# Optimization experiments

Hardware: AMD Instinct MI355X
Metric: run time of the kernel (lower is better)

## Reference

```python
import jax, jax.numpy as jnp
import numpy as np

D = 512      # emb_size
H = 8        # attention heads
E = 8        # num experts
HID = 512    # expert MLP hidden (assumed StandardExpert = 2-layer MLP)
NTOK = 8192  # 8*1024 tokens
W_IMP = 0.01


def setup_inputs() -> dict:
    key = jax.random.key(0)
    ks = jax.random.split(key, 16)
    f = lambda i, shape, s=0.02: (jax.random.normal(ks[i], shape, jnp.float32) * s)
    return {
        "x": jax.random.normal(ks[0], (8, 1024, D), jnp.float32),
        "q": jax.random.normal(ks[1], (NTOK, D), jnp.float32),
        "Wq": f(2, (D, D)), "bq": jnp.zeros((D,), jnp.float32),
        "Wk": f(3, (D, D)), "bk": jnp.zeros((D,), jnp.float32),
        "Wv": f(4, (D, D)), "bv": jnp.zeros((D,), jnp.float32),
        "Wo": f(5, (D, D)), "bo": jnp.zeros((D,), jnp.float32),
        "gate_W": f(6, (D, E)), "gate_b": jnp.zeros((E,), jnp.float32),
        "W1": f(7, (E, D, HID)), "b1": jnp.zeros((E, HID), jnp.float32),
        "W2": f(8, (E, HID, D)), "b2": jnp.zeros((E, D), jnp.float32),
        "top": 2,
    }


def _cross_att(xf, q, Wq, bq, Wk, bk, Wv, bv, Wo, bo):
    # seq_len == 1 on both sides after unsqueeze(1) in the torch code
    N, d = xf.shape
    dh = d // H
    Q = (xf @ Wq + bq).reshape(N, H, dh)
    K = (q @ Wk + bk).reshape(N, H, dh)
    V = (q @ Wv + bv).reshape(N, H, dh)
    scores = jnp.sum(Q * K, axis=-1, keepdims=True) / jnp.sqrt(jnp.float32(dh))  # [N,H,1]
    w = jax.nn.softmax(scores, axis=-1)  # trivially ones (single key), kept for fidelity
    att = (w * V).reshape(N, d)
    return att @ Wo + bo


def reference(x, q, Wq, bq, Wk, bk, Wv, bv, Wo, bo, gate_W, gate_b, W1, b1, W2, b2, top):
    x_shape = x.shape
    xf = x.reshape(-1, x_shape[-1])  # [N, D]
    att = _cross_att(xf, q, Wq, bq, Wk, bk, Wv, bv, Wo, bo)
    gate_logits = att @ gate_W + gate_b
    gate_prob = jax.nn.softmax(gate_logits, axis=-1)  # [N, E] (eval mode: no noise)
    top_w, top_i = jax.lax.top_k(gate_prob, top)       # [N, top]
    top_w = jax.nn.softmax(top_w, axis=-1)
    # combine weights per expert: comb[n,e] = sum_k top_w[n,k] * [top_i[n,k]==e]
    comb = jnp.sum(top_w[..., None] * jax.nn.one_hot(top_i, E, dtype=xf.dtype), axis=1)  # [N, E]
    y = jnp.zeros_like(xf)
    for e in range(E):  # fixed small expert loop; dense compute + mask-combine
        h = jax.nn.relu(xf @ W1[e] + b1[e])
        ye = h @ W2[e] + b2[e]
        y = y + comb[:, e:e + 1] * ye
    importance = gate_prob.sum(axis=0)  # [E]
    # torch.std uses ddof=1
    importance_loss = W_IMP * (jnp.std(importance, ddof=1) / jnp.mean(importance)) ** 2
    return y.reshape(x_shape), gate_prob, importance_loss
```

## Files before the change

kernel.cpp:

```cpp
#include <hip/hip_runtime.h>
#include <math.h>
#include <stdint.h>

#define NTOK 8192
#define DIM  512
#define NEXP 8
#define HIDN 512
#define BM 128
#define BN 128
#define BK 32
#define MAXRB 72
#define SLOTS (MAXRB*BM)
#define GBLK (NTOK/16)

typedef _Float16 f16;
typedef __attribute__((ext_vector_type(4))) _Float16 f16x4;
typedef __attribute__((ext_vector_type(8))) _Float16 f16x8;
typedef __attribute__((ext_vector_type(4))) float    f32x4;

__device__ __forceinline__ void gl2lds16(const void* g, void* l) {
  __builtin_amdgcn_global_load_lds(
      (const __attribute__((address_space(1))) unsigned int*)(g),
      (__attribute__((address_space(3))) unsigned int*)(l), 16, 0, 0);
}

__global__ __launch_bounds__(256) void k_prep(
    const float* __restrict__ x, f16* __restrict__ xh,
    const float* __restrict__ W1, const float* __restrict__ W2,
    f16* __restrict__ W1t, f16* __restrict__ W2t) {
  const int bx = blockIdx.x, tid = threadIdx.x;
  if (bx < 4096) {
    int i4 = (bx * 256 + tid) * 4;
    float4 v = *(const float4*)(x + i4);
    f16x4 o; o.x = (_Float16)v.x; o.y = (_Float16)v.y; o.z = (_Float16)v.z; o.w = (_Float16)v.w;
    *(f16x4*)(xh + i4) = o;
  } else {
    __shared__ float t[32][33];
    int idx = bx - 4096;
    int z = idx >> 8, rem = idx & 255;
    int k0 = (rem >> 4) * 32, n0 = (rem & 15) * 32;
    const float* src = (z < 8 ? W1 : W2) + (size_t)(z & 7) * DIM * DIM;
    f16* dst = (z < 8 ? W1t : W2t) + (size_t)(z & 7) * DIM * DIM;
    int tx = tid & 31, ty = tid >> 5;
    for (int r = ty; r < 32; r += 8) t[r][tx] = src[(size_t)(k0 + r) * DIM + n0 + tx];
    __syncthreads();
    for (int r = ty; r < 32; r += 8) dst[(size_t)(n0 + r) * DIM + k0 + tx] = (f16)t[tx][r];
  }
}

__global__ void k_foldA(const float* __restrict__ Wo, const float* __restrict__ gW,
                        double* __restrict__ G1) {
  int out = blockIdx.x * 4 + (threadIdx.x >> 6);
  int lane = threadIdx.x & 63;
  int d = out >> 3, e = out & 7;
  double acc = 0.0;
#pragma unroll
  for (int j = 0; j < 8; j++) {
    int k = j * 64 + lane;
    acc += (double)Wo[d * DIM + k] * (double)gW[k * NEXP + e];
  }
#pragma unroll
  for (int off = 32; off; off >>= 1) acc += __shfl_xor(acc, off, 64);
  if (lane == 0) G1[out] = acc;
}

__global__ void k_foldB(const float* __restrict__ Wv, const double* __restrict__ G1,
                        float* __restrict__ Wg, const float* __restrict__ bv,
                        const float* __restrict__ bo, const float* __restrict__ gW,
                        const float* __restrict__ gb, double* __restrict__ bg) {
  int lane = threadIdx.x & 63;
  if (blockIdx.x == 1024) {
    int w = threadIdx.x >> 6;
    for (int e = w; e < NEXP; e += 4) {
      double acc = 0.0;
#pragma unroll
      for (int j = 0; j < 8; j++) {
        int d = j * 64 + lane;
        acc += (double)bv[d] * G1[d * NEXP + e] + (double)bo[d] * (double)gW[d * NEXP + e];
      }
#pragma unroll
      for (int off = 32; off; off >>= 1) acc += __shfl_xor(acc, off, 64);
      if (lane == 0) bg[e] = acc + (double)gb[e];
    }
    return;
  }
  int out = blockIdx.x * 4 + (threadIdx.x >> 6);
  int d = out >> 3, e = out & 7;
  double acc = 0.0;
#pragma unroll
  for (int j = 0; j < 8; j++) {
    int k = j * 64 + lane;
    acc += (double)Wv[d * DIM + k] * G1[k * NEXP + e];
  }
#pragma unroll
  for (int off = 32; off; off >>= 1) acc += __shfl_xor(acc, off, 64);
  if (lane == 0) Wg[out] = (float)acc;
}

__global__ __launch_bounds__(256) void k_gate(
    const float* __restrict__ q, const float* __restrict__ Wg,
    const double* __restrict__ bg, float* __restrict__ gp_out,
    int* __restrict__ e1a, int* __restrict__ e2a,
    float* __restrict__ w1a, float* __restrict__ w2a,
    int* __restrict__ r1a, int* __restrict__ r2a, int* __restrict__ hist,
    float* __restrict__ gpsum) {
  __shared__ float qs[16 * 513];
  __shared__ float ps[16][8];
  __shared__ int cnt[16];
  const int tid = threadIdx.x;
  const int tok0 = blockIdx.x * 16;

  for (int i = tid; i < 16 * 512; i += 256) {
    int r = i >> 9, c = i & 511;
    qs[r * 513 + c] = q[(size_t)(tok0 + r) * DIM + c];
  }
  if (tid < 16) cnt[tid] = 0;
  __syncthreads();

  const int e = tid & 7;
  const int half = (tid >> 3) & 1;
  const int tl = tid >> 4;
  const float* qrow = qs + tl * 513 + half * 256;
  const float* wcol = Wg + half * 256 * NEXP + e;

  double a0 = 0, a1 = 0, a2 = 0, a3 = 0;
#pragma unroll 4
  for (int j = 0; j < 256; j += 4) {
    a0 += (double)qrow[j]     * (double)wcol[(size_t)j * NEXP];
    a1 += (double)qrow[j + 1] * (double)wcol[(size_t)(j + 1) * NEXP];
    a2 += (double)qrow[j + 2] * (double)wcol[(size_t)(j + 2) * NEXP];
    a3 += (double)qrow[j + 3] * (double)wcol[(size_t)(j + 3) * NEXP];
  }
  double acc = (a0 + a1) + (a2 + a3);
  acc += __shfl_xor(acc, 8, 64);

  double l = acc + bg[e];
  double m = l;
#pragma unroll
  for (int off = 1; off < 8; off <<= 1) m = fmax(m, __shfl_xor(m, off, 64));
  float ex = expf((float)(l - m));
  float s = ex;
#pragma unroll
  for (int off = 1; off < 8; off <<= 1) s += __shfl_xor(s, off, 64);
  float pf = ex / s;
  int tok = tok0 + tl;
  if (half == 0) { gp_out[(size_t)tok * NEXP + e] = pf; ps[tl][e] = pf; }

  double v1 = l; int i1 = e;
#pragma unroll
  for (int off = 1; off < 8; off <<= 1) {
    double ov = __shfl_xor(v1, off, 64);
    int oi = __shfl_xor(i1, off, 64);
    if (ov > v1 || (ov == v1 && oi < i1)) { v1 = ov; i1 = oi; }
  }
  double v2 = (e == i1) ? -1e300 : l; int i2 = e;
#pragma unroll
  for (int off = 1; off < 8; off <<= 1) {
    double ov = __shfl_xor(v2, off, 64);
    int oi = __shfl_xor(i2, off, 64);
    if (ov > v2 || (ov == v2 && oi < i2)) { v2 = ov; i2 = oi; }
  }
  float p1 = __shfl(pf, (tl << 4) + i1, 64);
  float p2 = __shfl(pf, (tl << 4) + i2, 64);
  if (e == 0 && half == 0) {
    float ev = expf(p2 - p1);
    float iw = 1.0f / (1.0f + ev);
    e1a[tok] = i1; e2a[tok] = i2;
    w1a[tok] = iw; w2a[tok] = ev * iw;
    r1a[tok] = atomicAdd(&cnt[i1], 1);
    r2a[tok] = atomicAdd(&cnt[8 + i2], 1);
  }
  __syncthreads();
  if (tid < 16) hist[blockIdx.x * 16 + tid] = cnt[tid];
  if (tid < 8) {
    float ssum = 0.f;
#pragma unroll
    for (int r = 0; r < 16; r++) ssum += ps[r][tid];
    gpsum[blockIdx.x * 8 + tid] = ssum;
  }
}

__global__ __launch_bounds__(1024) void k_scan2(const int* __restrict__ hist,
                                                int* __restrict__ blockbase,
                                                int* __restrict__ aoff,
                                                int* __restrict__ counts,
                                                int* __restrict__ toks,
                                                const float* __restrict__ gpsum,
                                                float* __restrict__ loss) {
  __shared__ int tot[16];
  __shared__ int s_ao[16];
  __shared__ double imp[8];
  const int c = threadIdx.x >> 6;
  const int l = threadIdx.x & 63;
  int v[GBLK / 64];
  int s = 0;
#pragma unroll
  for (int j = 0; j < GBLK / 64; j++) {
    v[j] = hist[((l * (GBLK / 64) + j) << 4) + c];
    s += v[j];
  }
  int incl = s;
#pragma unroll
  for (int off = 1; off < 64; off <<= 1) {
    int t = __shfl_up(incl, off, 64);
    if (l >= off) incl += t;
  }
  int run = incl - s;
#pragma unroll
  for (int j = 0; j < GBLK / 64; j++) {
    blockbase[((l * (GBLK / 64) + j) << 4) + c] = run;
    run += v[j];
  }
  if (l == 63) tot[c] = incl;
  __syncthreads();
  if (threadIdx.x == 0) {
    int o0 = 0, o1 = 0;
    for (int e = 0; e < NEXP; e++) {
      counts[e] = tot[e];
      aoff[e] = o0; s_ao[e] = o0; o0 += (tot[e] + BM - 1) / BM * BM;
      counts[8 + e] = tot[8 + e];
      aoff[9 + e] = o1; s_ao[8 + e] = o1; o1 += (tot[8 + e] + BM - 1) / BM * BM;
    }
    aoff[8] = o0; aoff[17] = o1;
  }
  __syncthreads();
  const int cnt_c = tot[c];
  const int padded = (cnt_c + BM - 1) / BM * BM;
  const int base = ((c >> 3) ? SLOTS : 0) + s_ao[c];
  for (int sidx = cnt_c + l; sidx < padded; sidx += 64)
    toks[base + sidx] = 0;
  if (c < 8) {
    double a = 0.0;
#pragma unroll
    for (int j = 0; j < GBLK / 64; j++)
      a += (double)gpsum[(size_t)(l + j * 64) * 8 + c];
#pragma unroll
    for (int off = 32; off; off >>= 1) a += __shfl_xor(a, off, 64);
    if (l == 0) imp[c] = a;
  }
  __syncthreads();
  if (threadIdx.x == 0) {
    double mn = 0.0;
    for (int e = 0; e < 8; e++) mn += imp[e];
    mn *= (1.0 / 8.0);
    double var = 0.0;
    for (int e = 0; e < 8; e++) { double d = imp[e] - mn; var += d * d; }
    var *= (1.0 / 7.0);
    double r = sqrt(var) / mn;
    loss[0] = (float)(0.01 * r * r);
  }
}

__global__ void k_scatter2(const int* __restrict__ e1a, const int* __restrict__ e2a,
                           const float* __restrict__ w1a, const float* __restrict__ w2a,
                           const int* __restrict__ r1a, const int* __restrict__ r2a,
                           const int* __restrict__ blockbase, const int* __restrict__ aoff,
                           int* __restrict__ toks, float* __restrict__ wsl) {
  int n = blockIdx.x * 256 + threadIdx.x;
  int blk = n >> 4;
  int e1 = e1a[n];
  int slot = aoff[e1] + blockbase[(blk << 4) + e1] + r1a[n];
  toks[slot] = n; wsl[slot] = w1a[n];
  int e2 = e2a[n];
  slot = SLOTS + aoff[9 + e2] + blockbase[(blk << 4) + 8 + e2] + r2a[n];
  toks[slot] = n; wsl[slot] = w2a[n];
}

template <int MODE>
__global__ __launch_bounds__(256) void k_expert(
    const f16* __restrict__ Asrc, const f16* __restrict__ Wt,
    const float* __restrict__ bias, const int* __restrict__ toks,
    const float* __restrict__ wsl, const int* __restrict__ aoff,
    const int* __restrict__ counts, f16* __restrict__ Hout,
    float* __restrict__ y) {
  const int klist = (MODE == 0) ? blockIdx.z : (MODE == 2 ? 1 : 0);
  const int* ao = aoff + klist * 9;
  const int slot0 = blockIdx.x * BM;
  if (slot0 >= ao[8]) return;
  int e = 0;
#pragma unroll
  for (int t = 1; t <= 7; t++) if (slot0 >= ao[t]) e = t;

  const int n0 = blockIdx.y * BN;
  const int tid = threadIdx.x, lane = tid & 63, wid = tid >> 6;

  __shared__ __align__(16) f16 As[BM * BK];
  __shared__ __align__(16) f16 Bs[BN * BK];

  const int srow = wid * 16 + (lane >> 2);
  const int scol = (lane & 3) * 8;
  const f16* arow[2];
  const f16* brow[2];
  f16* alds[2];
  f16* blds[2];
#pragma unroll
  for (int rnd = 0; rnd < 2; rnd++) {
    int r = srow + rnd * 64;
    if (MODE == 0) {
      int tk = toks[klist * SLOTS + slot0 + r];
      arow[rnd] = Asrc + (size_t)tk * DIM + scol;
    } else {
      arow[rnd] = Asrc + (size_t)(klist * SLOTS + slot0 + r) * HIDN + scol;
    }
    brow[rnd] = Wt + ((size_t)e * DIM + n0 + r) * DIM + scol;
    alds[rnd] = As + (wid * 16 + rnd * 64) * BK;
    blds[rnd] = Bs + (wid * 16 + rnd * 64) * BK;
  }

  f32x4 acc[4][4] = {};
  const int wr = wid >> 1, wc = wid & 1;
  const int fr = lane & 15, kb = (lane >> 4) * 8;

  for (int ks = 0; ks < DIM; ks += BK) {
    __syncthreads();
#pragma unroll
    for (int rnd = 0; rnd < 2; rnd++) {
      gl2lds16(arow[rnd] + ks, alds[rnd]);
      gl2lds16(brow[rnd] + ks, blds[rnd]);
    }
    __syncthreads();
    f16x8 af[4], bf[4];
#pragma unroll
    for (int m = 0; m < 4; m++)
      af[m] = *(const f16x8*)(As + (wr * 64 + m * 16 + fr) * BK + kb);
#pragma unroll
    for (int n = 0; n < 4; n++)
      bf[n] = *(const f16x8*)(Bs + (wc * 64 + n * 16 + fr) * BK + kb);
#pragma unroll
    for (int m = 0; m < 4; m++)
#pragma unroll
      for (int n = 0; n < 4; n++)
        acc[m][n] = __builtin_amdgcn_mfma_f32_16x16x32_f16(af[m], bf[n], acc[m][n], 0, 0, 0);
  }

  float bcol[4];
#pragma unroll
  for (int n = 0; n < 4; n++)
    bcol[n] = bias[e * ((MODE == 0) ? HIDN : DIM) + n0 + wc * 64 + n * 16 + fr];

  if (MODE == 0) {
#pragma unroll
    for (int m = 0; m < 4; m++)
#pragma unroll
      for (int r4 = 0; r4 < 4; r4++) {
        int slot = slot0 + wr * 64 + m * 16 + (lane >> 4) * 4 + r4;
#pragma unroll
        for (int n = 0; n < 4; n++) {
          int col = n0 + wc * 64 + n * 16 + fr;
          float v = acc[m][n][r4] + bcol[n];
          Hout[(size_t)(klist * SLOTS + slot) * HIDN + col] = (f16)fmaxf(v, 0.f);
        }
      }
  } else {
    const int vend = ao[e] + counts[klist * 8 + e];
#pragma unroll
    for (int m = 0; m < 4; m++)
#pragma unroll
      for (int r4 = 0; r4 < 4; r4++) {
        int slot = slot0 + wr * 64 + m * 16 + (lane >> 4) * 4 + r4;
        if (slot < vend) {
          int tk = toks[klist * SLOTS + slot];
          float w = wsl[klist * SLOTS + slot];
#pragma unroll
          for (int n = 0; n < 4; n++) {
            int col = n0 + wc * 64 + n * 16 + fr;
            float v = (acc[m][n][r4] + bcol[n]) * w;
            size_t oi = (size_t)tk * DIM + col;
            if (MODE == 1) y[oi] = v;
            else y[oi] += v;
          }
        }
      }
  }
}

extern "C" void kernel_launch(void* const* d_in, const int* in_sizes, int n_in,
                              void* d_out, int out_size, void* d_ws, size_t ws_size,
                              hipStream_t stream) {
  const float* x  = (const float*)d_in[0];
  const float* q  = (const float*)d_in[1];
  const float* Wv = (const float*)d_in[6];
  const float* bv = (const float*)d_in[7];
  const float* Wo = (const float*)d_in[8];
  const float* bo = (const float*)d_in[9];
  const float* gW = (const float*)d_in[10];
  const float* gb = (const float*)d_in[11];
  const float* W1 = (const float*)d_in[12];
  const float* b1 = (const float*)d_in[13];
  const float* W2 = (const float*)d_in[14];
  const float* b2 = (const float*)d_in[15];

  float* out = (float*)d_out;
  float* y_out = out;
  float* gp_out = out + (size_t)NTOK * DIM;
  float* loss_out = gp_out + (size_t)NTOK * NEXP;

  uint8_t* w = (uint8_t*)d_ws;
  size_t o = 0;
  auto alloc = [&](size_t bytes) -> void* {
    void* p = w + o;
    o = (o + bytes + 255) & ~(size_t)255;
    return p;
  };
  f16* xh      = (f16*)alloc((size_t)NTOK * DIM * 2);
  f16* W1t     = (f16*)alloc((size_t)NEXP * DIM * HIDN * 2);
  f16* W2t     = (f16*)alloc((size_t)NEXP * DIM * HIDN * 2);
  f16* Hbuf    = (f16*)alloc((size_t)2 * SLOTS * HIDN * 2);
  double* G1   = (double*)alloc((size_t)DIM * NEXP * 8);
  float* Wg    = (float*)alloc((size_t)DIM * NEXP * 4);
  double* bg   = (double*)alloc(NEXP * 8);
  int* e1a     = (int*)alloc(NTOK * 4);
  int* e2a     = (int*)alloc(NTOK * 4);
  float* w1a   = (float*)alloc(NTOK * 4);
  float* w2a   = (float*)alloc(NTOK * 4);
  int* r1a     = (int*)alloc(NTOK * 4);
  int* r2a     = (int*)alloc(NTOK * 4);
  int* hist    = (int*)alloc((size_t)GBLK * 16 * 4);
  int* bbase   = (int*)alloc((size_t)GBLK * 16 * 4);
  float* gpsum = (float*)alloc((size_t)GBLK * 8 * 4);
  int* counts  = (int*)alloc(16 * 4);
  int* aoff    = (int*)alloc(18 * 4);
  int* toks    = (int*)alloc((size_t)2 * SLOTS * 4);
  float* wsl   = (float*)alloc((size_t)2 * SLOTS * 4);
  (void)ws_size; (void)in_sizes; (void)n_in; (void)out_size;

  k_prep<<<8192, 256, 0, stream>>>(x, xh, W1, W2, W1t, W2t);
  k_foldA<<<1024, 256, 0, stream>>>(Wo, gW, G1);
  k_foldB<<<1025, 256, 0, stream>>>(Wv, G1, Wg, bv, bo, gW, gb, bg);
  k_gate<<<GBLK, 256, 0, stream>>>(q, Wg, bg, gp_out, e1a, e2a, w1a, w2a, r1a, r2a, hist, gpsum);
  k_scan2<<<1, 1024, 0, stream>>>(hist, bbase, aoff, counts, toks, gpsum, loss_out);
  k_scatter2<<<NTOK / 256, 256, 0, stream>>>(e1a, e2a, w1a, w2a, r1a, r2a, bbase, aoff, toks, wsl);
  k_expert<0><<<dim3(MAXRB, 4, 2), 256, 0, stream>>>(xh, W1t, b1, toks, wsl, aoff, counts,
                                                     Hbuf, nullptr);
  k_expert<1><<<dim3(MAXRB, 4, 1), 256, 0, stream>>>(Hbuf, W2t, b2, toks, wsl, aoff, counts,
                                                     nullptr, y_out);
  k_expert<2><<<dim3(MAXRB, 4, 1), 256, 0, stream>>>(Hbuf, W2t, b2, toks, wsl, aoff, counts,
                                                     nullptr, y_out);
}
```

Before: 116.7 us.

## Use k-chunked LDS layout with BK=64, transposed MFMA, vectorized epilogue, fuse foldA

```diff
diff --git a/kernel.cpp b/kernel.cpp
--- a/kernel.cpp
+++ b/kernel.cpp
@@ -8,7 +8,7 @@
 #define HIDN 512
 #define BM 128
 #define BN 128
-#define BK 32
+#define BK 64
 #define MAXRB 72
 #define SLOTS (MAXRB*BM)
 #define GBLK (NTOK/16)
@@ -27,14 +27,16 @@
 __global__ __launch_bounds__(256) void k_prep(
     const float* __restrict__ x, f16* __restrict__ xh,
     const float* __restrict__ W1, const float* __restrict__ W2,
-    f16* __restrict__ W1t, f16* __restrict__ W2t) {
+    f16* __restrict__ W1t, f16* __restrict__ W2t,
+    const float* __restrict__ Wo, const float* __restrict__ gW,
+    double* __restrict__ G1) {
   const int bx = blockIdx.x, tid = threadIdx.x;
   if (bx < 4096) {
     int i4 = (bx * 256 + tid) * 4;
     float4 v = *(const float4*)(x + i4);
     f16x4 o; o.x = (_Float16)v.x; o.y = (_Float16)v.y; o.z = (_Float16)v.z; o.w = (_Float16)v.w;
     *(f16x4*)(xh + i4) = o;
-  } else {
+  } else if (bx < 8192) {
     __shared__ float t[32][33];
     int idx = bx - 4096;
     int z = idx >> 8, rem = idx & 255;
@@ -45,23 +47,20 @@
     for (int r = ty; r < 32; r += 8) t[r][tx] = src[(size_t)(k0 + r) * DIM + n0 + tx];
     __syncthreads();
     for (int r = ty; r < 32; r += 8) dst[(size_t)(n0 + r) * DIM + k0 + tx] = (f16)t[tx][r];
-  }
-}
-
-__global__ void k_foldA(const float* __restrict__ Wo, const float* __restrict__ gW,
-                        double* __restrict__ G1) {
-  int out = blockIdx.x * 4 + (threadIdx.x >> 6);
-  int lane = threadIdx.x & 63;
-  int d = out >> 3, e = out & 7;
-  double acc = 0.0;
-#pragma unroll
-  for (int j = 0; j < 8; j++) {
-    int k = j * 64 + lane;
-    acc += (double)Wo[d * DIM + k] * (double)gW[k * NEXP + e];
-  }
-#pragma unroll
-  for (int off = 32; off; off >>= 1) acc += __shfl_xor(acc, off, 64);
-  if (lane == 0) G1[out] = acc;
+  } else {
+    int out = (bx - 8192) * 4 + (tid >> 6);
+    int lane = tid & 63;
+    int d = out >> 3, e = out & 7;
+    double acc = 0.0;
+#pragma unroll
+    for (int j = 0; j < 8; j++) {
+      int k = j * 64 + lane;
+      acc += (double)Wo[d * DIM + k] * (double)gW[k * NEXP + e];
+    }
+#pragma unroll
+    for (int off = 32; off; off >>= 1) acc += __shfl_xor(acc, off, 64);
+    if (lane == 0) G1[out] = acc;
+  }
 }
 
 __global__ void k_foldB(const float* __restrict__ Wv, const double* __restrict__ G1,
@@ -284,93 +283,104 @@
   const int n0 = blockIdx.y * BN;
   const int tid = threadIdx.x, lane = tid & 63, wid = tid >> 6;
 
-  __shared__ __align__(16) f16 As[BM * BK];
-  __shared__ __align__(16) f16 Bs[BN * BK];
-
-  const int srow = wid * 16 + (lane >> 2);
-  const int scol = (lane & 3) * 8;
-  const f16* arow[2];
-  const f16* brow[2];
-  f16* alds[2];
-  f16* blds[2];
-#pragma unroll
-  for (int rnd = 0; rnd < 2; rnd++) {
-    int r = srow + rnd * 64;
+  __shared__ __align__(16) f16 As[8 * 128 * 8];
+  __shared__ __align__(16) f16 Bs[8 * 128 * 8];
+
+  const f16* abase[2];
+  const f16* bbase[2];
+#pragma unroll
+  for (int half = 0; half < 2; half++) {
+    int row = half * 64 + lane;
     if (MODE == 0) {
-      int tk = toks[klist * SLOTS + slot0 + r];
-      arow[rnd] = Asrc + (size_t)tk * DIM + scol;
+      int tk = toks[klist * SLOTS + slot0 + row];
+      abase[half] = Asrc + (size_t)tk * DIM;
     } else {
-      arow[rnd] = Asrc + (size_t)(klist * SLOTS + slot0 + r) * HIDN + scol;
-    }
-    brow[rnd] = Wt + ((size_t)e * DIM + n0 + r) * DIM + scol;
-    alds[rnd] = As + (wid * 16 + rnd * 64) * BK;
-    blds[rnd] = Bs + (wid * 16 + rnd * 64) * BK;
+      abase[half] = Asrc + (size_t)(klist * SLOTS + slot0 + row) * HIDN;
+    }
+    bbase[half] = Wt + ((size_t)e * DIM + n0 + row) * DIM;
   }
 
   f32x4 acc[4][4] = {};
   const int wr = wid >> 1, wc = wid & 1;
-  const int fr = lane & 15, kb = (lane >> 4) * 8;
+  const int fr = lane & 15, hi2 = lane >> 4;
 
   for (int ks = 0; ks < DIM; ks += BK) {
     __syncthreads();
 #pragma unroll
-    for (int rnd = 0; rnd < 2; rnd++) {
-      gl2lds16(arow[rnd] + ks, alds[rnd]);
-      gl2lds16(brow[rnd] + ks, blds[rnd]);
+    for (int q = 0; q < 2; q++) {
+      const int kc = wid * 2 + q;
+#pragma unroll
+      for (int half = 0; half < 2; half++) {
+        gl2lds16(abase[half] + ks + kc * 8, As + kc * 1024 + half * 512);
+        gl2lds16(bbase[half] + ks + kc * 8, Bs + kc * 1024 + half * 512);
+      }
     }
     __syncthreads();
-    f16x8 af[4], bf[4];
-#pragma unroll
-    for (int m = 0; m < 4; m++)
-      af[m] = *(const f16x8*)(As + (wr * 64 + m * 16 + fr) * BK + kb);
-#pragma unroll
-    for (int n = 0; n < 4; n++)
-      bf[n] = *(const f16x8*)(Bs + (wc * 64 + n * 16 + fr) * BK + kb);
-#pragma unroll
-    for (int m = 0; m < 4; m++)
+#pragma unroll
+    for (int w2 = 0; w2 < 2; w2++) {
+      const int kc = w2 * 4 + hi2;
+      f16x8 af[4], bf[4];
+#pragma unroll
+      for (int m = 0; m < 4; m++)
+        af[m] = *(const f16x8*)(As + kc * 1024 + (wr * 64 + m * 16 + fr) * 8);
 #pragma unroll
       for (int n = 0; n < 4; n++)
-        acc[m][n] = __builtin_amdgcn_mfma_f32_16x16x32_f16(af[m], bf[n], acc[m][n], 0, 0, 0);
-  }
-
-  float bcol[4];
-#pragma unroll
-  for (int n = 0; n < 4; n++)
-    bcol[n] = bias[e * ((MODE == 0) ? HIDN : DIM) + n0 + wc * 64 + n * 16 + fr];
-
+        bf[n] = *(const f16x8*)(Bs + kc * 1024 + (wc * 64 + n * 16 + fr) * 8);
+#pragma unroll
+      for (int m = 0; m < 4; m++)
+#pragma unroll
+        for (int n = 0; n < 4; n++)
+          acc[n][m] = __builtin_amdgcn_mfma_f32_16x16x32_f16(bf[n], af[m], acc[n][m], 0, 0, 0);
+    }
+  }
+
+  const int bstride = (MODE == 0) ? HIDN : DIM;
   if (MODE == 0) {
 #pragma unroll
-    for (int m = 0; m < 4; m++)
-#pragma unroll
-      for (int r4 = 0; r4 < 4; r4++) {
-        int slot = slot0 + wr * 64 + m * 16 + (lane >> 4) * 4 + r4;
-#pragma unroll
-        for (int n = 0; n < 4; n++) {
-          int col = n0 + wc * 64 + n * 16 + fr;
-          float v = acc[m][n][r4] + bcol[n];
-          Hout[(size_t)(klist * SLOTS + slot) * HIDN + col] = (f16)fmaxf(v, 0.f);
-        }
+    for (int m = 0; m < 4; m++) {
+      const int slot = slot0 + wr * 64 + m * 16 + fr;
+      const size_t hrow = (size_t)(klist * SLOTS + slot) * HIDN;
+#pragma unroll
+      for (int n = 0; n < 4; n++) {
+        const int col0 = n0 + wc * 64 + n * 16 + hi2 * 4;
+        float4 b4 = *(const float4*)(bias + e * bstride + col0);
+        f16x4 hv;
+        hv[0] = (f16)fmaxf(acc[n][m][0] + b4.x, 0.f);
+        hv[1] = (f16)fmaxf(acc[n][m][1] + b4.y, 0.f);
+        hv[2] = (f16)fmaxf(acc[n][m][2] + b4.z, 0.f);
+        hv[3] = (f16)fmaxf(acc[n][m][3] + b4.w, 0.f);
+        *(f16x4*)(Hout + hrow + col0) = hv;
       }
+    }
   } else {
     const int vend = ao[e] + counts[klist * 8 + e];
 #pragma unroll
-    for (int m = 0; m < 4; m++)
-#pragma unroll
-      for (int r4 = 0; r4 < 4; r4++) {
-        int slot = slot0 + wr * 64 + m * 16 + (lane >> 4) * 4 + r4;
-        if (slot < vend) {
-          int tk = toks[klist * SLOTS + slot];
-          float w = wsl[klist * SLOTS + slot];
-#pragma unroll
-          for (int n = 0; n < 4; n++) {
-            int col = n0 + wc * 64 + n * 16 + fr;
-            float v = (acc[m][n][r4] + bcol[n]) * w;
-            size_t oi = (size_t)tk * DIM + col;
-            if (MODE == 1) y[oi] = v;
-            else y[oi] += v;
+    for (int m = 0; m < 4; m++) {
+      const int slot = slot0 + wr * 64 + m * 16 + fr;
+      if (slot < vend) {
+        const int tk = toks[klist * SLOTS + slot];
+        const float w = wsl[klist * SLOTS + slot];
+        const size_t yrow = (size_t)tk * DIM;
+#pragma unroll
+        for (int n = 0; n < 4; n++) {
+          const int col0 = n0 + wc * 64 + n * 16 + hi2 * 4;
+          float4 b4 = *(const float4*)(bias + e * bstride + col0);
+          float4 v;
+          v.x = (acc[n][m][0] + b4.x) * w;
+          v.y = (acc[n][m][1] + b4.y) * w;
+          v.z = (acc[n][m][2] + b4.z) * w;
+          v.w = (acc[n][m][3] + b4.w) * w;
+          float* yp = y + yrow + col0;
+          if (MODE == 1) {
+            *(float4*)yp = v;
+          } else {
+            float4 old = *(const float4*)yp;
+            v.x += old.x; v.y += old.y; v.z += old.z; v.w += old.w;
+            *(float4*)yp = v;
           }
         }
       }
+    }
   }
 }
 
@@ -424,8 +434,7 @@
   float* wsl   = (float*)alloc((size_t)2 * SLOTS * 4);
   (void)ws_size; (void)in_sizes; (void)n_in; (void)out_size;
 
-  k_prep<<<8192, 256, 0, stream>>>(x, xh, W1, W2, W1t, W2t);
-  k_foldA<<<1024, 256, 0, stream>>>(Wo, gW, G1);
+  k_prep<<<9216, 256, 0, stream>>>(x, xh, W1, W2, W1t, W2t, Wo, gW, G1);
   k_foldB<<<1025, 256, 0, stream>>>(Wv, G1, Wg, bv, bo, gW, gb, bg);
   k_gate<<<GBLK, 256, 0, stream>>>(q, Wg, bg, gp_out, e1a, e2a, w1a, w2a, r1a, r2a, hist, gpsum);
   k_scan2<<<1, 1024, 0, stream>>>(hist, bbase, aoff, counts, toks, gpsum, loss_out);
```

Result: slower. 147.3 us (+26.2%).
